# Kernel optimization log

Hardware: AMD Instinct MI355X
Metric: run time of the kernel (lower is better)

## Reference

```python
import jax, jax.numpy as jnp
import numpy as np

EPS = 1e-5
NEG_INF = -1e30


def layer_norm_seq(x, gamma, beta):
    # Faithful to the custom LayerNorm: normalizes over dim=1 (the T axis of
    # [B, T, C]) with UNBIASED variance (torch.var default), then scales by
    # gamma/beta of shape [C] broadcast over the last axis.
    m = jnp.mean(x, axis=1, keepdims=True)
    v = jnp.var(x, axis=1, keepdims=True, ddof=1)
    return gamma * (x - m) / jnp.sqrt(v + EPS) + beta


def setup_inputs() -> dict:
    key = jax.random.key(0)
    B, T, C, H = 4, 1024, 1024, 16
    hd = C // H  # 64
    ks = jax.random.split(key, 10)
    s_in = 1.0 / np.sqrt(C)
    s_ff = 1.0 / np.sqrt(4 * C)
    return {
        "x": jax.random.normal(ks[0], (B, T, C), dtype=jnp.float32),
        # NOTE: Head uses self.key(x) for BOTH q and k; the query Linear is
        # dead code, so only key/value weights are materialized.
        "Wk": jax.random.uniform(ks[1], (H, C, hd), minval=-s_in, maxval=s_in, dtype=jnp.float32),
        "Wv": jax.random.uniform(ks[2], (H, C, hd), minval=-s_in, maxval=s_in, dtype=jnp.float32),
        "Wp": jax.random.uniform(ks[3], (C, C), minval=-s_in, maxval=s_in, dtype=jnp.float32),
        "bp": jnp.zeros((C,), dtype=jnp.float32),
        "W1": jax.random.uniform(ks[4], (4 * C, C), minval=-s_in, maxval=s_in, dtype=jnp.float32),
        "b1": jnp.zeros((4 * C,), dtype=jnp.float32),
        "W2": jax.random.uniform(ks[5], (C, 4 * C), minval=-s_ff, maxval=s_ff, dtype=jnp.float32),
        "b2": jnp.zeros((C,), dtype=jnp.float32),
        "g1": jnp.ones((C,), dtype=jnp.float32),
        "beta1": jnp.zeros((C,), dtype=jnp.float32),
        "g2": jnp.ones((C,), dtype=jnp.float32),
        "beta2": jnp.zeros((C,), dtype=jnp.float32),
    }


def reference(x, Wk, Wv, Wp, bp, W1, b1, W2, b2, g1, beta1, g2, beta2):
    B, T, C = x.shape
    H, _, hd = Wk.shape
    scale = hd ** -0.5

    # --- self-attention sublayer (pre-LN over sequence axis) ---
    h = layer_norm_seq(x, g1, beta1)
    # q and k BOTH use the key projection (faithful to the original bug).
    qk = jnp.einsum("btc,hcd->bhtd", h, Wk)          # [B,H,T,hd]
    v = jnp.einsum("btc,hcd->bhtd", h, Wv)           # [B,H,T,hd]
    wei = jnp.einsum("bhtd,bhsd->bhts", qk, qk) * scale  # [B,H,T,T]
    causal = jnp.tril(jnp.ones((T, T), dtype=bool))
    wei = jnp.where(causal, wei, NEG_INF)
    wei = jax.nn.softmax(wei, axis=-1)
    attn = jnp.einsum("bhts,bhsd->bthd", wei, v).reshape(B, T, C)
    attn = attn @ Wp.T + bp
    x = x + attn

    # --- feed-forward sublayer ---
    h2 = layer_norm_seq(x, g2, beta2)
    ff = jax.nn.relu(h2 @ W1.T + b1) @ W2.T + b2
    return x + ff
```

## Files before the change

### kernel.cpp

```cpp
#include <hip/hip_runtime.h>
#include <stdint.h>


#define BDIM 256

typedef __attribute__((ext_vector_type(8))) __bf16 bf16x8;
typedef __attribute__((ext_vector_type(4))) float f32x4;

__device__ __forceinline__ unsigned short f2bf(float f) {
    unsigned u = __float_as_uint(f);
    u += 0x7fff + ((u >> 16) & 1);
    return (unsigned short)(u >> 16);
}

__device__ __forceinline__ void gload_lds16(const void* g, void* l) {
    __builtin_amdgcn_global_load_lds(
        (const __attribute__((address_space(1))) void*)g,
        (__attribute__((address_space(3))) void*)l, 16, 0, 0);
}

__global__ void k_cast_bf16(const float* __restrict__ in, unsigned short* __restrict__ out, int n4) {
    int i = blockIdx.x * BDIM + threadIdx.x;
    if (i >= n4) return;
    float4 v = ((const float4*)in)[i];
    ushort4 o;
    o.x = f2bf(v.x); o.y = f2bf(v.y); o.z = f2bf(v.z); o.w = f2bf(v.w);
    ((ushort4*)out)[i] = o;
}

__global__ void k_headT(const float* __restrict__ W, unsigned short* __restrict__ out) {
    __shared__ float tile[64][65];
    const int tid = threadIdx.x;
    const int c0 = blockIdx.x * 64, h = blockIdx.y;
    const float* src = W + ((long)h << 16) + (long)c0 * 64;
    #pragma unroll
    for (int j = 0; j < 16; ++j) {
        int idx = j * 256 + tid;
        tile[idx >> 6][idx & 63] = src[idx];
    }
    __syncthreads();
    #pragma unroll
    for (int j = 0; j < 16; ++j) {
        int idx = j * 256 + tid;
        int d = idx >> 6, c = idx & 63;
        out[(long)(h * 64 + d) * 1024 + c0 + c] = f2bf(tile[c][d]);
    }
}

__global__ void k_ln_part(const float* __restrict__ x, float* __restrict__ psum, float* __restrict__ psq) {
    int c = blockIdx.x * BDIM + threadIdx.x;
    int tc = blockIdx.y, b = blockIdx.z;
    const float* p = x + ((long)b << 20) + ((long)tc * 128) * 1024 + c;
    float s = 0.f, ss = 0.f;
    for (int t = 0; t < 128; ++t) {
        float v = p[t * 1024];
        s += v; ss += v * v;
    }
    int o = (b * 8 + tc) * 1024 + c;
    psum[o] = s; psq[o] = ss;
}

__global__ void k_ln_fin(const float* __restrict__ psum, const float* __restrict__ psq,
                         float* __restrict__ mean, float* __restrict__ rstd) {
    int i = blockIdx.x * BDIM + threadIdx.x;
    int b = i >> 10, c = i & 1023;
    float s = 0.f, ss = 0.f;
    for (int j = 0; j < 8; ++j) {
        s  += psum[(b * 8 + j) * 1024 + c];
        ss += psq[(b * 8 + j) * 1024 + c];
    }
    float m = s * (1.0f / 1024.0f);
    float var = (ss - 1024.0f * m * m) * (1.0f / 1023.0f);
    mean[i] = m;
    rstd[i] = rsqrtf(var + 1e-5f);
}

__global__ void k_ln_apply(const float* __restrict__ x, const float* __restrict__ mean,
                           const float* __restrict__ rstd, const float* __restrict__ g,
                           const float* __restrict__ beta, unsigned short* __restrict__ out) {
    int i = blockIdx.x * BDIM + threadIdx.x;
    int flat = i << 2;
    int b = flat >> 20, c = flat & 1023;
    float4 xv = ((const float4*)x)[i];
    float4 mv = *(const float4*)&mean[(b << 10) + c];
    float4 rv = *(const float4*)&rstd[(b << 10) + c];
    float4 gv = *(const float4*)&g[c];
    float4 bv = *(const float4*)&beta[c];
    ushort4 o;
    o.x = f2bf(gv.x * (xv.x - mv.x) * rv.x + bv.x);
    o.y = f2bf(gv.y * (xv.y - mv.y) * rv.y + bv.y);
    o.z = f2bf(gv.z * (xv.z - mv.z) * rv.z + bv.z);
    o.w = f2bf(gv.w * (xv.w - mv.w) * rv.w + bv.w);
    ((ushort4*)out)[i] = o;
}

__global__ void k_addbias(const float* __restrict__ res, const float* __restrict__ bias,
                          float* __restrict__ out) {
    int i = blockIdx.x * BDIM + threadIdx.x;
    int c = (i << 2) & 1023;
    float4 r = ((const float4*)res)[i];
    float4 bv = *(const float4*)&bias[c];
    r.x += bv.x; r.y += bv.y; r.z += bv.z; r.w += bv.w;
    ((float4*)out)[i] = r;
}

template <int EPI>
__global__ __launch_bounds__(256, 2) void k_gemm_bt(
    const unsigned short* __restrict__ A, const unsigned short* __restrict__ B,
    void* __restrict__ Cv, const float* __restrict__ bias, const float* __restrict__ res,
    int N, int K, int ldA, int ldB, long sA, long sB, long sC)
{
    __shared__ __align__(16) unsigned short As[2][128 * 64];
    __shared__ __align__(16) unsigned short Bs[2][128 * 64];
    const int tid = threadIdx.x;
    const int wv = tid >> 6, l = tid & 63;
    const long bz = blockIdx.z;

    const int gx = gridDim.x;
    const int nwg = gx * gridDim.y;
    int lin = blockIdx.y * gx + blockIdx.x;
    lin = (lin & 7) * (nwg >> 3) + (lin >> 3);
    const int m0 = (lin / gx) * 128, n0 = (lin % gx) * 128;

    const int lr = l & 15, lg = l >> 4;

    const int srow = wv * 32 + (l >> 3);
    const unsigned short* pA = A + bz * sA + (long)(m0 + srow) * ldA;
    const unsigned short* pB = B + bz * sB + (long)(n0 + srow) * ldB;

    auto stage = [&](int k0, int d) {
        #pragma unroll
        for (int L = 0; L < 4; ++L) {
            const int g = ((l & 7) ^ ((L * 4 + (l >> 4)) & 7)) * 8;
            gload_lds16(pA + (long)(L * 8) * ldA + k0 + g, &As[d][(wv * 4 + L) * 512]);
            gload_lds16(pB + (long)(L * 8) * ldB + k0 + g, &Bs[d][(wv * 4 + L) * 512]);
        }
    };

    f32x4 acc[4][4] = {};
    const int wm = (wv >> 1) * 64, wn = (wv & 1) * 64;
    const int rsw = (lr >> 1) & 7;

    const int nt = K >> 6;
    stage(0, 0);
    asm volatile("s_waitcnt vmcnt(0)" ::: "memory");
    __builtin_amdgcn_s_barrier();
    __builtin_amdgcn_sched_barrier(0);

    for (int t = 0; t < nt; ++t) {
        const int d = t & 1;
        if (t + 1 < nt) stage((t + 1) << 6, d ^ 1);
        #pragma unroll
        for (int ks = 0; ks < 2; ++ks) {
            bf16x8 af[4], bfr[4];
            #pragma unroll
            for (int fm = 0; fm < 4; ++fm)
                af[fm] = *(const bf16x8*)&As[d][(wm + fm * 16 + lr) * 64 + (((ks * 4 + lg) ^ rsw) * 8)];
            #pragma unroll
            for (int fn = 0; fn < 4; ++fn)
                bfr[fn] = *(const bf16x8*)&Bs[d][(wn + fn * 16 + lr) * 64 + (((ks * 4 + lg) ^ rsw) * 8)];
            asm volatile("s_waitcnt lgkmcnt(0)" ::: "memory");
            __builtin_amdgcn_sched_barrier(0);
            __builtin_amdgcn_s_setprio(1);
            #pragma unroll
            for (int fm = 0; fm < 4; ++fm)
                #pragma unroll
                for (int fn = 0; fn < 4; ++fn)
                    acc[fm][fn] = __builtin_amdgcn_mfma_f32_16x16x32_bf16(af[fm], bfr[fn], acc[fm][fn], 0, 0, 0);
            __builtin_amdgcn_s_setprio(0);
            __builtin_amdgcn_sched_barrier(0);
        }
        asm volatile("s_waitcnt vmcnt(0)" ::: "memory");
        __builtin_amdgcn_s_barrier();
        __builtin_amdgcn_sched_barrier(0);
    }

    const int cr0 = lg * 4;
    #pragma unroll
    for (int fm = 0; fm < 4; ++fm) {
        #pragma unroll
        for (int r = 0; r < 4; ++r) {
            const int row = m0 + wm + fm * 16 + cr0 + r;
            const long rb = bz * sC + (long)row * N;
            #pragma unroll
            for (int fn = 0; fn < 4; ++fn) {
                const int col = n0 + wn + fn * 16 + lr;
                float v = acc[fm][fn][r];
                if (EPI == 0) {
                    ((unsigned short*)Cv)[rb + col] = f2bf(v);
                } else if (EPI == 1) {
                    ((float*)Cv)[rb + col] = v + bias[col] + res[rb + col];
                } else if (EPI == 2) {
                    v += bias[col];
                    ((unsigned short*)Cv)[rb + col] = f2bf(v > 0.f ? v : 0.f);
                } else {
                    atomicAdd(&((float*)Cv)[rb + col], v);
                }
            }
        }
    }
}

#define CEXP 0.18033688f
#define PSTRIDE 72

__global__ __launch_bounds__(256, 2) void k_attn(
    const unsigned short* __restrict__ qk, const unsigned short* __restrict__ vt,
    unsigned short* __restrict__ ctx)
{
    __shared__ __align__(16) unsigned short Ks[64 * 64];
    __shared__ __align__(16) unsigned short Vs[64 * 64];
    __shared__ __align__(16) unsigned short P[4][16 * PSTRIDE];
    const int tid = threadIdx.x;
    const int wave = tid >> 6, lane = tid & 63;
    const int bh = blockIdx.x >> 3, pairIdx = blockIdx.x & 7;
    const int b = bh >> 4, h = bh & 15;
    const int lr = lane & 15, lg = lane >> 4;

    const int swz = (lr & 7) << 4;
    const int cby0 = (lg * 16) ^ swz;
    const int cby1 = (64 + lg * 16) ^ swz;
    const int srow_l = lane >> 3;
    const int scol = ((lane & 7) * 8) ^ (srow_l << 3);

    unsigned short* Pw = P[wave];
    char* KsB = (char*)Ks;
    char* VsB = (char*)Vs;
    const unsigned short* qbase = qk + ((long)b << 20) + h * 64;
    const unsigned short* vb    = vt + ((long)(b * 16 + h) << 16);

    #pragma unroll 1
    for (int phase = 0; phase < 2; ++phase) {
        const int qb = phase ? (15 - pairIdx) : pairIdx;
        const int q0 = qb << 6;
        const int qw = q0 + wave * 16;

        const unsigned short* qrow = qbase + (long)(qw + lr) * 1024 + lg * 8;
        const bf16x8 aq0 = *(const bf16x8*)qrow;
        const bf16x8 aq1 = *(const bf16x8*)(qrow + 32);

        f32x4 acc[4] = {};
        float mrow[4] = {-1e30f, -1e30f, -1e30f, -1e30f};
        float lrow[4] = {0.f, 0.f, 0.f, 0.f};

        for (int c = 0; c <= qb; ++c) {
            const int k0 = c << 6;
            __syncthreads();
            #pragma unroll
            for (int i = 0; i < 2; ++i) {
                const int row = i * 32 + wave * 8 + srow_l;
                gload_lds16(qbase + (long)(k0 + row) * 1024 + scol,
                            KsB + i * 4096 + wave * 1024);
                gload_lds16(vb + (long)row * 1024 + k0 + scol,
                            VsB + i * 4096 + wave * 1024);
            }
            __syncthreads();

            f32x4 s[4];
            #pragma unroll
            for (int t = 0; t < 4; ++t) {
                const int r = t * 16 + lr;
                bf16x8 bk0 = *(const bf16x8*)(KsB + r * 128 + cby0);
                bf16x8 bk1 = *(const bf16x8*)(KsB + r * 128 + cby1);
                f32x4 z = {};
                z = __builtin_amdgcn_mfma_f32_16x16x32_bf16(aq0, bk0, z, 0, 0, 0);
                s[t] = __builtin_amdgcn_mfma_f32_16x16x32_bf16(aq1, bk1, z, 0, 0, 0);
            }
            if (c == qb) {
                #pragma unroll
                for (int t = 0; t < 4; ++t) {
                    const int col = t * 16 + lr;
                    #pragma unroll
                    for (int r = 0; r < 4; ++r)
                        if (col > wave * 16 + lg * 4 + r) s[t][r] = -1e30f;
                }
            }
            float fac[4];
            #pragma unroll
            for (int r = 0; r < 4; ++r) {
                float v = fmaxf(fmaxf(s[0][r], s[1][r]), fmaxf(s[2][r], s[3][r]));
                v = fmaxf(v, __shfl_xor(v, 1));
                v = fmaxf(v, __shfl_xor(v, 2));
                v = fmaxf(v, __shfl_xor(v, 4));
                v = fmaxf(v, __shfl_xor(v, 8));
                float mn = fmaxf(mrow[r], v);
                fac[r] = exp2f((mrow[r] - mn) * CEXP);
                mrow[r] = mn;
            }
            float psum[4] = {0.f, 0.f, 0.f, 0.f};
            #pragma unroll
            for (int t = 0; t < 4; ++t) {
                #pragma unroll
                for (int r = 0; r < 4; ++r) {
                    float p = exp2f((s[t][r] - mrow[r]) * CEXP);
                    psum[r] += p;
                    Pw[(lg * 4 + r) * PSTRIDE + t * 16 + lr] = f2bf(p);
                }
            }
            #pragma unroll
            for (int r = 0; r < 4; ++r) {
                float v = psum[r];
                v += __shfl_xor(v, 1); v += __shfl_xor(v, 2);
                v += __shfl_xor(v, 4); v += __shfl_xor(v, 8);
                lrow[r] = lrow[r] * fac[r] + v;
            }
            #pragma unroll
            for (int ni = 0; ni < 4; ++ni)
                #pragma unroll
                for (int r = 0; r < 4; ++r)
                    acc[ni][r] *= fac[r];
            const bf16x8 pa0 = *(const bf16x8*)&Pw[lr * PSTRIDE + lg * 8];
            const bf16x8 pa1 = *(const bf16x8*)&Pw[lr * PSTRIDE + 32 + lg * 8];
            #pragma unroll
            for (int ni = 0; ni < 4; ++ni) {
                const int vr = ni * 16 + lr;
                bf16x8 bv0 = *(const bf16x8*)(VsB + vr * 128 + cby0);
                bf16x8 bv1 = *(const bf16x8*)(VsB + vr * 128 + cby1);
                acc[ni] = __builtin_amdgcn_mfma_f32_16x16x32_bf16(pa0, bv0, acc[ni], 0, 0, 0);
                acc[ni] = __builtin_amdgcn_mfma_f32_16x16x32_bf16(pa1, bv1, acc[ni], 0, 0, 0);
            }
        }

        unsigned short* crow = ctx + ((long)(b * 1024 + qw)) * 1024 + h * 64;
        #pragma unroll
        for (int r = 0; r < 4; ++r) {
            const float inv = 1.0f / lrow[r];
            #pragma unroll
            for (int ni = 0; ni < 4; ++ni)
                crow[(long)(lg * 4 + r) * 1024 + ni * 16 + lr] = f2bf(acc[ni][r] * inv);
        }
    }
}

extern "C" void kernel_launch(void* const* d_in, const int* in_sizes, int n_in,
                              void* d_out, int out_size, void* d_ws, size_t ws_size,
                              hipStream_t stream)
{
    const float* x   = (const float*)d_in[0];
    const float* Wk  = (const float*)d_in[1];
    const float* Wv  = (const float*)d_in[2];
    const float* Wp  = (const float*)d_in[3];
    const float* bp  = (const float*)d_in[4];
    const float* W1  = (const float*)d_in[5];
    const float* b1  = (const float*)d_in[6];
    const float* W2  = (const float*)d_in[7];
    const float* b2  = (const float*)d_in[8];
    const float* g1  = (const float*)d_in[9];
    const float* be1 = (const float*)d_in[10];
    const float* g2  = (const float*)d_in[11];
    const float* be2 = (const float*)d_in[12];
    float* out = (float*)d_out;

    char* ws = (char*)d_ws;
    const long MB = 1024 * 1024;
    unsigned short* BkT = (unsigned short*)(ws);
    unsigned short* WvT = (unsigned short*)(ws + 2 * MB);
    unsigned short* WpB = (unsigned short*)(ws + 4 * MB);
    unsigned short* W1B = (unsigned short*)(ws + 6 * MB);
    unsigned short* W2B = (unsigned short*)(ws + 14 * MB);
    unsigned short* hB  = (unsigned short*)(ws + 22 * MB);
    unsigned short* qkB = (unsigned short*)(ws + 30 * MB);
    unsigned short* VtB = (unsigned short*)(ws + 38 * MB);
    unsigned short* ctx = (unsigned short*)(ws + 46 * MB);
    unsigned short* ff1 = (unsigned short*)(ws + 30 * MB);
    float* x2   = (float*)(ws + 62 * MB);
    float* psum = (float*)(ws + 78 * MB);
    float* psq  = (float*)(ws + 78 * MB + 128 * 1024);
    float* mean = (float*)(ws + 78 * MB + 256 * 1024);
    float* rstd = (float*)(ws + 78 * MB + 272 * 1024);

    k_cast_bf16<<<1024, BDIM, 0, stream>>>(Wp, WpB, 262144);
    k_cast_bf16<<<4096, BDIM, 0, stream>>>(W1, W1B, 1048576);
    k_cast_bf16<<<4096, BDIM, 0, stream>>>(W2, W2B, 1048576);
    k_headT<<<dim3(16, 16), BDIM, 0, stream>>>(Wk, BkT);
    k_headT<<<dim3(16, 16), BDIM, 0, stream>>>(Wv, WvT);

    k_ln_part<<<dim3(4, 8, 4), BDIM, 0, stream>>>(x, psum, psq);
    k_ln_fin<<<16, BDIM, 0, stream>>>(psum, psq, mean, rstd);
    k_ln_apply<<<4096, BDIM, 0, stream>>>(x, mean, rstd, g1, be1, hB);

    k_gemm_bt<0><<<dim3(8, 32, 1), BDIM, 0, stream>>>(hB, BkT, qkB, nullptr, nullptr, 1024, 1024, 1024, 1024, 0, 0, 0);
    k_gemm_bt<0><<<dim3(8, 8, 4), BDIM, 0, stream>>>(WvT, hB, VtB, nullptr, nullptr, 1024, 1024, 1024, 1024, 0, MB, MB);

    k_attn<<<512, BDIM, 0, stream>>>(qkB, VtB, ctx);

    k_gemm_bt<1><<<dim3(8, 32, 1), BDIM, 0, stream>>>(ctx, WpB, x2, bp, x, 1024, 1024, 1024, 1024, 0, 0, 0);

    k_ln_part<<<dim3(4, 8, 4), BDIM, 0, stream>>>(x2, psum, psq);
    k_ln_fin<<<16, BDIM, 0, stream>>>(psum, psq, mean, rstd);
    k_ln_apply<<<4096, BDIM, 0, stream>>>(x2, mean, rstd, g2, be2, hB);

    k_gemm_bt<2><<<dim3(32, 32, 1), BDIM, 0, stream>>>(hB, W1B, ff1, b1, nullptr, 4096, 1024, 1024, 1024, 0, 0, 0);

    k_addbias<<<4096, BDIM, 0, stream>>>(x2, b2, out);
    k_gemm_bt<3><<<dim3(8, 32, 2), BDIM, 0, stream>>>(ff1, W2B, out, nullptr, nullptr, 1024, 2048, 4096, 4096, 2048, 2048, 0);
}
```

Baseline: 366.1 us.

## Software-pipeline LDS fragment loads in GEMM and double-buffer K/V tiles in attention

The GEMM main loop now prefetches the first k-half fragments for the next tile after the barrier and loads the second k-half fragments while the first half's MFMAs run, so LDS reads overlap matrix math. The attention kernel double-buffers its K and V shared-memory tiles and issues the global-to-LDS loads for the next key block before computing on the current one, so a chunk needs one barrier instead of two and memory latency is hidden. In exchange, attention LDS use roughly doubles, which may lower occupancy, and the GEMM holds more fragment registers.

```diff
diff --git a/kernel.cpp b/kernel.cpp
--- a/kernel.cpp
+++ b/kernel.cpp
@@ -140,6 +140,8 @@
     f32x4 acc[4][4] = {};
     const int wm = (wv >> 1) * 64, wn = (wv & 1) * 64;
     const int rsw = (lr >> 1) & 7;
+    const int ob0 = ((0 + lg) ^ rsw) * 8;
+    const int ob1 = ((4 + lg) ^ rsw) * 8;
 
     const int nt = K >> 6;
     stage(0, 0);
@@ -147,32 +149,54 @@
     __builtin_amdgcn_s_barrier();
     __builtin_amdgcn_sched_barrier(0);
 
+    bf16x8 afA[4], bfA[4];
+    #pragma unroll
+    for (int fm = 0; fm < 4; ++fm)
+        afA[fm] = *(const bf16x8*)&As[0][(wm + fm * 16 + lr) * 64 + ob0];
+    #pragma unroll
+    for (int fn = 0; fn < 4; ++fn)
+        bfA[fn] = *(const bf16x8*)&Bs[0][(wn + fn * 16 + lr) * 64 + ob0];
+
     for (int t = 0; t < nt; ++t) {
         const int d = t & 1;
         if (t + 1 < nt) stage((t + 1) << 6, d ^ 1);
-        #pragma unroll
-        for (int ks = 0; ks < 2; ++ks) {
-            bf16x8 af[4], bfr[4];
-            #pragma unroll
-            for (int fm = 0; fm < 4; ++fm)
-                af[fm] = *(const bf16x8*)&As[d][(wm + fm * 16 + lr) * 64 + (((ks * 4 + lg) ^ rsw) * 8)];
+        asm volatile("s_waitcnt lgkmcnt(0)" ::: "memory");
+        __builtin_amdgcn_sched_barrier(0);
+        bf16x8 afB[4], bfB[4];
+        #pragma unroll
+        for (int fm = 0; fm < 4; ++fm)
+            afB[fm] = *(const bf16x8*)&As[d][(wm + fm * 16 + lr) * 64 + ob1];
+        #pragma unroll
+        for (int fn = 0; fn < 4; ++fn)
+            bfB[fn] = *(const bf16x8*)&Bs[d][(wn + fn * 16 + lr) * 64 + ob1];
+        __builtin_amdgcn_s_setprio(1);
+        #pragma unroll
+        for (int fm = 0; fm < 4; ++fm)
             #pragma unroll
             for (int fn = 0; fn < 4; ++fn)
-                bfr[fn] = *(const bf16x8*)&Bs[d][(wn + fn * 16 + lr) * 64 + (((ks * 4 + lg) ^ rsw) * 8)];
-            asm volatile("s_waitcnt lgkmcnt(0)" ::: "memory");
-            __builtin_amdgcn_sched_barrier(0);
-            __builtin_amdgcn_s_setprio(1);
-            #pragma unroll
-            for (int fm = 0; fm < 4; ++fm)
-                #pragma unroll
-                for (int fn = 0; fn < 4; ++fn)
-                    acc[fm][fn] = __builtin_amdgcn_mfma_f32_16x16x32_bf16(af[fm], bfr[fn], acc[fm][fn], 0, 0, 0);
-            __builtin_amdgcn_s_setprio(0);
-            __builtin_amdgcn_sched_barrier(0);
-        }
+                acc[fm][fn] = __builtin_amdgcn_mfma_f32_16x16x32_bf16(afA[fm], bfA[fn], acc[fm][fn], 0, 0, 0);
+        __builtin_amdgcn_s_setprio(0);
+        asm volatile("s_waitcnt lgkmcnt(0)" ::: "memory");
+        __builtin_amdgcn_sched_barrier(0);
+        __builtin_amdgcn_s_setprio(1);
+        #pragma unroll
+        for (int fm = 0; fm < 4; ++fm)
+            #pragma unroll
+            for (int fn = 0; fn < 4; ++fn)
+                acc[fm][fn] = __builtin_amdgcn_mfma_f32_16x16x32_bf16(afB[fm], bfB[fn], acc[fm][fn], 0, 0, 0);
+        __builtin_amdgcn_s_setprio(0);
+        __builtin_amdgcn_sched_barrier(0);
         asm volatile("s_waitcnt vmcnt(0)" ::: "memory");
         __builtin_amdgcn_s_barrier();
         __builtin_amdgcn_sched_barrier(0);
+        if (t + 1 < nt) {
+            #pragma unroll
+            for (int fm = 0; fm < 4; ++fm)
+                afA[fm] = *(const bf16x8*)&As[d ^ 1][(wm + fm * 16 + lr) * 64 + ob0];
+            #pragma unroll
+            for (int fn = 0; fn < 4; ++fn)
+                bfA[fn] = *(const bf16x8*)&Bs[d ^ 1][(wn + fn * 16 + lr) * 64 + ob0];
+        }
     }
 
     const int cr0 = lg * 4;
@@ -208,8 +232,8 @@
     const unsigned short* __restrict__ qk, const unsigned short* __restrict__ vt,
     unsigned short* __restrict__ ctx)
 {
-    __shared__ __align__(16) unsigned short Ks[64 * 64];
-    __shared__ __align__(16) unsigned short Vs[64 * 64];
+    __shared__ __align__(16) unsigned short Ks[2][64 * 64];
+    __shared__ __align__(16) unsigned short Vs[2][64 * 64];
     __shared__ __align__(16) unsigned short P[4][16 * PSTRIDE];
     const int tid = threadIdx.x;
     const int wave = tid >> 6, lane = tid & 63;
@@ -243,25 +267,36 @@
         float mrow[4] = {-1e30f, -1e30f, -1e30f, -1e30f};
         float lrow[4] = {0.f, 0.f, 0.f, 0.f};
 
+        __syncthreads();
+        #pragma unroll
+        for (int i = 0; i < 2; ++i) {
+            const int row = i * 32 + wave * 8 + srow_l;
+            gload_lds16(qbase + (long)row * 1024 + scol, KsB + i * 4096 + wave * 1024);
+            gload_lds16(vb + (long)row * 1024 + scol, VsB + i * 4096 + wave * 1024);
+        }
+
         for (int c = 0; c <= qb; ++c) {
-            const int k0 = c << 6;
-            __syncthreads();
-            #pragma unroll
-            for (int i = 0; i < 2; ++i) {
-                const int row = i * 32 + wave * 8 + srow_l;
-                gload_lds16(qbase + (long)(k0 + row) * 1024 + scol,
-                            KsB + i * 4096 + wave * 1024);
-                gload_lds16(vb + (long)row * 1024 + k0 + scol,
-                            VsB + i * 4096 + wave * 1024);
-            }
-            __syncthreads();
+            const int dB = (c & 1) << 13;
+            asm volatile("s_waitcnt vmcnt(0)" ::: "memory");
+            __builtin_amdgcn_s_barrier();
+            __builtin_amdgcn_sched_barrier(0);
+            if (c < qb) {
+                const int k1 = (c + 1) << 6;
+                const int dN = ((c + 1) & 1) << 13;
+                #pragma unroll
+                for (int i = 0; i < 2; ++i) {
+                    const int row = i * 32 + wave * 8 + srow_l;
+                    gload_lds16(qbase + (long)(k1 + row) * 1024 + scol, KsB + dN + i * 4096 + wave * 1024);
+                    gload_lds16(vb + (long)row * 1024 + k1 + scol, VsB + dN + i * 4096 + wave * 1024);
+                }
+            }
 
             f32x4 s[4];
             #pragma unroll
             for (int t = 0; t < 4; ++t) {
                 const int r = t * 16 + lr;
-                bf16x8 bk0 = *(const bf16x8*)(KsB + r * 128 + cby0);
-                bf16x8 bk1 = *(const bf16x8*)(KsB + r * 128 + cby1);
+                bf16x8 bk0 = *(const bf16x8*)(KsB + dB + r * 128 + cby0);
+                bf16x8 bk1 = *(const bf16x8*)(KsB + dB + r * 128 + cby1);
                 f32x4 z = {};
                 z = __builtin_amdgcn_mfma_f32_16x16x32_bf16(aq0, bk0, z, 0, 0, 0);
                 s[t] = __builtin_amdgcn_mfma_f32_16x16x32_bf16(aq1, bk1, z, 0, 0, 0);
@@ -314,8 +349,8 @@
             #pragma unroll
             for (int ni = 0; ni < 4; ++ni) {
                 const int vr = ni * 16 + lr;
-                bf16x8 bv0 = *(const bf16x8*)(VsB + vr * 128 + cby0);
-                bf16x8 bv1 = *(const bf16x8*)(VsB + vr * 128 + cby1);
+                bf16x8 bv0 = *(const bf16x8*)(VsB + dB + vr * 128 + cby0);
+                bf16x8 bv1 = *(const bf16x8*)(VsB + dB + vr * 128 + cby1);
                 acc[ni] = __builtin_amdgcn_mfma_f32_16x16x32_bf16(pa0, bv0, acc[ni], 0, 0, 0);
                 acc[ni] = __builtin_amdgcn_mfma_f32_16x16x32_bf16(pa1, bv1, acc[ni], 0, 0, 0);
             }
```

Result: no change. 366.2 us (+0.0%).
